# Optimization experiments

Measured on AMD Instinct MI355X. Metric: run time of the kernel, lower is better.

## Reference

```python
import jax, jax.numpy as jnp
import numpy as np

B, T, E, D, N, L, NF = 4, 2048, 512, 512, 16, 4, 2048


def setup_inputs() -> dict:
    key = jax.random.key(0)
    ks = jax.random.split(key, 12)
    r = lambda k, s, sc=1.0: jax.random.normal(k, s, dtype=jnp.float32) * sc
    return {
        "text_emb": r(ks[0], (B, T, E)),
        "W_in": r(ks[1], (E, D), 1.0 / np.sqrt(E).astype(np.float32)),
        "b_in": jnp.zeros((D,), jnp.float32),
        "freq_pe": r(ks[2], (NF, D), 0.02),
        # diagonal-SSM (S4D) params per layer, stacked on leading L axis
        "A_log": r(ks[3], (L, D, N), 0.5),
        "B_ssm": r(ks[4], (L, D, N), 0.5),
        "C_ssm": r(ks[5], (L, D, N), 0.5),
        "log_dt": r(ks[6], (L, D), 0.5) - 4.6,  # dt ~ 0.01
        "D_skip": r(ks[7], (L, D), 0.5),
        "ln_f0_scale": jnp.ones((D,), jnp.float32),
        "ln_f0_bias": jnp.zeros((D,), jnp.float32),
        "W_f0": r(ks[8], (D, 1), 1.0 / np.sqrt(D).astype(np.float32)),
        "b_f0": jnp.zeros((1,), jnp.float32),
        "ln_en_scale": jnp.ones((D,), jnp.float32),
        "ln_en_bias": jnp.zeros((D,), jnp.float32),
        "W_en": r(ks[9], (D, 1), 1.0 / np.sqrt(D).astype(np.float32)),
        "b_en": jnp.zeros((1,), jnp.float32),
    }


def _layernorm(x, scale, bias, eps=1e-5):
    mu = jnp.mean(x, axis=-1, keepdims=True)
    var = jnp.mean(jnp.square(x - mu), axis=-1, keepdims=True)
    return (x - mu) * jax.lax.rsqrt(var + eps) * scale + bias


def _s4_layer(h, A_log, Bm, Cm, log_dt, Dsk):
    # h: [B, T, D]; diagonal SSM with ZOH discretization, scanned over T.
    dt = jnp.exp(log_dt)                 # [D]
    A = -jnp.exp(A_log)                  # [D, N], stable (negative real)
    Abar = jnp.exp(dt[:, None] * A)      # [D, N]
    Bbar = (Abar - 1.0) / A * Bm         # [D, N]
    u_t = jnp.transpose(h, (1, 0, 2))    # [T, B, D]
    x0 = jnp.zeros((h.shape[0], h.shape[2], A.shape[1]), h.dtype)  # [B, D, N]

    def step(x, u):
        x = Abar * x + Bbar * u[..., None]          # [B, D, N]
        y = jnp.einsum('bdn,dn->bd', x, Cm)         # readout
        return x, y

    _, ys = jax.lax.scan(step, x0, u_t)             # ys: [T, B, D]
    y = jnp.transpose(ys, (1, 0, 2)) + Dsk * h      # D skip connection
    return h + jax.nn.gelu(y)                       # residual + activation


def _forward(text_emb, W_in, b_in, freq_pe, A_log, B_ssm, C_ssm, log_dt,
             D_skip, ln_f0_scale, ln_f0_bias, W_f0, b_f0,
             ln_en_scale, ln_en_bias, W_en, b_en):
    x = text_emb @ W_in + b_in                      # [B, T, D]
    Tlen = x.shape[1]
    nf = freq_pe.shape[0]
    if nf >= Tlen:                                  # static-shape crop
        freq = freq_pe[:Tlen]
    else:                                           # static-shape edge pad
        pad = jnp.repeat(freq_pe[-1:], Tlen - nf, axis=0)
        freq = jnp.concatenate([freq_pe, pad], axis=0)
    h = x + freq[None, :, :]
    for l in range(A_log.shape[0]):
        h = _s4_layer(h, A_log[l], B_ssm[l], C_ssm[l], log_dt[l], D_skip[l])
    f0 = (_layernorm(h, ln_f0_scale, ln_f0_bias) @ W_f0 + b_f0)[..., 0]
    en = (_layernorm(h, ln_en_scale, ln_en_bias) @ W_en + b_en)[..., 0]
    return f0, en


def reference(text_emb, W_in, b_in, freq_pe, A_log, B_ssm, C_ssm, log_dt,
              D_skip, ln_f0_scale, ln_f0_bias, W_f0, b_f0,
              ln_en_scale, ln_en_bias, W_en, b_en):
    return _forward(text_emb, W_in, b_in, freq_pe, A_log, B_ssm, C_ssm,
                    log_dt, D_skip, ln_f0_scale, ln_f0_bias, W_f0, b_f0,
                    ln_en_scale, ln_en_bias, W_en, b_en)
```

## Files before the change

### kernel.cpp

```cpp
#include <hip/hip_runtime.h>

#define B_   4
#define T_   2048
#define E_   512
#define D_   512
#define N_   16
#define L_   4
#define TCH  16

typedef __bf16 bf16x8 __attribute__((ext_vector_type(8)));
typedef float  f32x4  __attribute__((ext_vector_type(4)));
typedef float  f32x2  __attribute__((ext_vector_type(2)));
typedef unsigned short us8 __attribute__((ext_vector_type(8)));

__device__ __forceinline__ float us2f(unsigned short u) {
    return __uint_as_float(((unsigned int)u) << 16);
}
__device__ __forceinline__ unsigned short f2us(float f) {
    unsigned int u = __float_as_uint(f);
    unsigned int r = (u + 0x7fffu + ((u >> 16) & 1u)) >> 16;
    return (unsigned short)r;
}
__device__ __forceinline__ float ldin(const void* p, int i, unsigned int f) {
    return f ? ((const float*)p)[i] : us2f(((const unsigned short*)p)[i]);
}
__device__ __forceinline__ unsigned int probe_f32(const void* lnfs) {
    return (((const unsigned int*)lnfs)[0] == 0x3F800000u) ? 1u : 0u;
}
__device__ __forceinline__ f32x2 pk_fma(f32x2 a, f32x2 b, f32x2 c) {
    f32x2 d;
    asm("v_pk_fma_f32 %0, %1, %2, %3" : "=v"(d) : "v"(a), "v"(b), "v"(c));
    return d;
}
__device__ __forceinline__ f32x2 pk_mul(f32x2 a, f32x2 b) {
    f32x2 d;
    asm("v_pk_mul_f32 %0, %1, %2" : "=v"(d) : "v"(a), "v"(b));
    return d;
}
template<int CTRL, int RM>
__device__ __forceinline__ f32x2 dpp2(f32x2 v) {
    f32x2 r;
    r[0] = __int_as_float(__builtin_amdgcn_update_dpp(0, __float_as_int(v[0]), CTRL, RM, 0xF, true));
    r[1] = __int_as_float(__builtin_amdgcn_update_dpp(0, __float_as_int(v[1]), CTRL, RM, 0xF, true));
    return r;
}

#define PA    0
#define PB    32768
#define PC    65536
#define PDT   98304
#define PDSK  100352
#define PLFS  102400
#define PLFB  102912
#define PWF   103424
#define PLES  103936
#define PLEB  104448
#define PWEN  104960
#define PSC   105472
#define PRM_N 105474

#define NB_TEXT 2048
#define NB_PRM  413
#define NB_WT   64
#define NB_S4P  128

__global__ __launch_bounds__(256) void prep_kernel(
    const void* X, const void* Win,
    const void* A_log, const void* B_ssm, const void* C_ssm,
    const void* log_dt, const void* D_skip,
    const void* lnfs, const void* lnfb, const void* Wf0,
    const void* lnes, const void* lneb, const void* Wen,
    const void* bf0, const void* ben,
    unsigned short* __restrict__ textc, unsigned short* __restrict__ Wt,
    float* __restrict__ P, float* __restrict__ P2) {
    __shared__ float tile[64 * 65];
    unsigned int f = probe_f32(lnfs);
    int bid = blockIdx.x;
    if (bid < NB_TEXT) {
        int i = (bid * 256 + threadIdx.x) * 8;
        if (f) {
            const float* xf = (const float*)X;
            us8 r;
#pragma unroll
            for (int j = 0; j < 8; j++) r[j] = f2us(xf[i + j]);
            *(us8*)(textc + i) = r;
        } else {
            *(us8*)(textc + i) = *(const us8*)((const unsigned short*)X + i);
        }
    } else if (bid < NB_TEXT + NB_PRM) {
        int i = (bid - NB_TEXT) * 256 + threadIdx.x;
        if      (i < PB)     P[i] = ldin(A_log,  i - PA,   f);
        else if (i < PC)     P[i] = ldin(B_ssm,  i - PB,   f);
        else if (i < PDT)    P[i] = ldin(C_ssm,  i - PC,   f);
        else if (i < PDSK)   P[i] = ldin(log_dt, i - PDT,  f);
        else if (i < PLFS)   P[i] = ldin(D_skip, i - PDSK, f);
        else if (i < PLFB)   P[i] = ldin(lnfs,   i - PLFS, f);
        else if (i < PWF)    P[i] = ldin(lnfb,   i - PLFB, f);
        else if (i < PLES)   P[i] = ldin(Wf0,    i - PWF,  f);
        else if (i < PLEB)   P[i] = ldin(lnes,   i - PLES, f);
        else if (i < PWEN)   P[i] = ldin(lneb,   i - PLEB, f);
        else if (i < PSC)    P[i] = ldin(Wen,    i - PWEN, f);
        else if (i == PSC)     P[i] = ldin(bf0, 0, f);
        else if (i == PSC + 1) P[i] = ldin(ben, 0, f);
    } else if (bid < NB_TEXT + NB_PRM + NB_WT) {
        int tb = bid - (NB_TEXT + NB_PRM);
        int d0 = (tb >> 3) * 64, e0 = (tb & 7) * 64;
        int r = threadIdx.x >> 6, i = threadIdx.x & 63;
#pragma unroll
        for (int k = 0; k < 16; k++) {
            int e = k * 4 + r;
            tile[e * 65 + i] = ldin(Win, (e0 + e) * D_ + d0 + i, f);
        }
        __syncthreads();
#pragma unroll
        for (int k = 0; k < 16; k++) {
            int dd = k * 4 + r;
            Wt[(size_t)(d0 + dd) * E_ + e0 + i] = f2us(tile[i * 65 + dd]);
        }
    } else {
        int i = (bid - (NB_TEXT + NB_PRM + NB_WT)) * 256 + threadIdx.x;
        int n = i & 15;
        int ld = i >> 4;
        float dt = __expf(ldin(log_dt, ld, f));
        float A  = -__expf(ldin(A_log, i, f));
        float Ab = __expf(dt * A);
        float Bb = (Ab - 1.f) / A * ldin(B_ssm, i, f);
        float l2M = 23.083120654223414f * dt * A;
        int base = ld * 64 + n;
        P2[base]      = Ab;
        P2[base + 16] = Bb * ldin(C_ssm, i, f);
        P2[base + 32] = exp2f(l2M);
        P2[base + 48] = l2M;
    }
}

__global__ __launch_bounds__(256) void gemm_kernel(const unsigned short* __restrict__ X,
                                                   const unsigned short* __restrict__ Wt,
                                                   const void* __restrict__ freq,
                                                   const void* __restrict__ b_in,
                                                   const void* __restrict__ lnfs,
                                                   float* __restrict__ H) {
    __shared__ unsigned short wlds[64 * 264];
    const unsigned int fl = probe_f32(lnfs);
    const int tid = threadIdx.x;
    const int w  = tid >> 6;
    const int ln = tid & 15;
    const int q  = (tid >> 4) & 3;
    const int d0 = blockIdx.x * 64;
    const int t0 = blockIdx.y * 128;
    const int b  = blockIdx.z;

    f32x4 acc[2][4];
#pragma unroll
    for (int i = 0; i < 2; i++)
#pragma unroll
        for (int j = 0; j < 4; j++) { acc[i][j][0]=0.f; acc[i][j][1]=0.f; acc[i][j][2]=0.f; acc[i][j][3]=0.f; }

    const size_t xbase = ((size_t)b * T_ + t0) * E_;

#pragma unroll
    for (int p = 0; p < 2; ++p) {
        if (p) __syncthreads();
#pragma unroll
        for (int it = 0; it < 8; ++it) {
            int flat = it * 256 + tid;
            int d = flat >> 5;
            int e = (flat & 31) << 3;
            bf16x8 v = *(const bf16x8*)(Wt + (size_t)(d0 + d) * E_ + p * 256 + e);
            *(bf16x8*)(wlds + d * 264 + e) = v;
        }
        __syncthreads();
#pragma unroll
        for (int s = 0; s < 8; ++s) {
            const int eo = s * 32 + q * 8;
            bf16x8 bfr[4];
#pragma unroll
            for (int j = 0; j < 4; j++)
                bfr[j] = *(const bf16x8*)(wlds + (j * 16 + ln) * 264 + eo);
#pragma unroll
            for (int sub = 0; sub < 2; ++sub) {
                const int t = w * 32 + sub * 16 + ln;
                bf16x8 afr = *(const bf16x8*)(X + xbase + (size_t)t * E_ + p * 256 + eo);
#pragma unroll
                for (int j = 0; j < 4; j++)
                    acc[sub][j] = __builtin_amdgcn_mfma_f32_16x16x32_bf16(afr, bfr[j], acc[sub][j], 0, 0, 0);
            }
        }
    }
#pragma unroll
    for (int sub = 0; sub < 2; ++sub) {
#pragma unroll
        for (int j = 0; j < 4; j++) {
            int d  = d0 + j * 16 + ln;
            int tb = t0 + w * 32 + sub * 16 + q * 4;
            float bi = ldin(b_in, d, fl);
            f32x4 o;
#pragma unroll
            for (int r4 = 0; r4 < 4; r4++)
                o[r4] = acc[sub][j][r4] + ldin(freq, (tb + r4) * D_ + d, fl) + bi;
            *(f32x4*)(H + ((size_t)b * D_ + d) * T_ + tb) = o;
        }
    }
}

__global__ __launch_bounds__(256) __attribute__((amdgpu_waves_per_eu(4, 4)))
void s4_kernel(float* __restrict__ H, const float* __restrict__ P,
               const float* __restrict__ P2) {
    __shared__ float hstate[2][2][16];
    const int w = threadIdx.x >> 6, lane = threadIdx.x & 63;
    const int rp = w >> 1, half = w & 1;
    const int row = blockIdx.x * 2 + rp;
    const int d = row & (D_ - 1);
    float* gp = H + (size_t)row * T_ + half * 1024 + lane * TCH;

    float u[TCH];
#pragma unroll
    for (int k = 0; k < 4; k++) {
        f32x4 v = *(const f32x4*)(gp + k * 4);
        u[k * 4] = v[0]; u[k * 4 + 1] = v[1]; u[k * 4 + 2] = v[2]; u[k * 4 + 3] = v[3];
    }

    for (int l = 0; l < L_; ++l) {
        const float* pp = P2 + (size_t)(((l << 9) + d) << 6);
        f32x2 Ab[8];
#pragma unroll
        for (int n = 0; n < 8; n++) Ab[n] = *(const f32x2*)(pp + 2 * n);
        f32x2 b[8];
#pragma unroll
        for (int n = 0; n < 8; n++) { b[n][0] = 0.f; b[n][1] = 0.f; }
#pragma unroll
        for (int j = 0; j < TCH; j++) {
            f32x2 u2; u2[0] = u[j]; u2[1] = u[j];
#pragma unroll
            for (int n = 0; n < 8; n++) b[n] = pk_fma(Ab[n], b[n], u2);
        }
        {
            f32x2 M1[8], w1[8], w2[8];
            float e1 = (float)((lane & 15) + 1);
            bool hi16 = (lane & 16) != 0;
#pragma unroll
            for (int n = 0; n < 8; n++) {
                M1[n] = *(const f32x2*)(pp + 32 + 2 * n);
                f32x2 l2m = *(const f32x2*)(pp + 48 + 2 * n);
                w1[n][0] = exp2f(l2m[0] * e1);  w1[n][1] = exp2f(l2m[1] * e1);
            }
#pragma unroll
            for (int n = 0; n < 8; n++) b[n] = pk_fma(M1[n], dpp2<0x111, 0xF>(b[n]), b[n]);
#pragma unroll
            for (int n = 0; n < 8; n++) M1[n] = pk_mul(M1[n], M1[n]);
#pragma unroll
            for (int n = 0; n < 8; n++) b[n] = pk_fma(M1[n], dpp2<0x112, 0xF>(b[n]), b[n]);
#pragma unroll
            for (int n = 0; n < 8; n++) M1[n] = pk_mul(M1[n], M1[n]);
#pragma unroll
            for (int n = 0; n < 8; n++) b[n] = pk_fma(M1[n], dpp2<0x114, 0xF>(b[n]), b[n]);
#pragma unroll
            for (int n = 0; n < 8; n++) M1[n] = pk_mul(M1[n], M1[n]);
#pragma unroll
            for (int n = 0; n < 8; n++) b[n] = pk_fma(M1[n], dpp2<0x118, 0xF>(b[n]), b[n]);
#pragma unroll
            for (int n = 0; n < 8; n++) {
                f32x2 M16 = pk_mul(M1[n], M1[n]);
                f32x2 wm  = pk_mul(w1[n], M16);
                w2[n][0] = hi16 ? wm[0] : w1[n][0];
                w2[n][1] = hi16 ? wm[1] : w1[n][1];
            }
#pragma unroll
            for (int n = 0; n < 8; n++) b[n] = pk_fma(w1[n], dpp2<0x142, 0xA>(b[n]), b[n]);
#pragma unroll
            for (int n = 0; n < 8; n++) b[n] = pk_fma(w2[n], dpp2<0x143, 0xC>(b[n]), b[n]);
        }
        if (half == 0 && lane == 63) {
#pragma unroll
            for (int n = 0; n < 8; n++) {
                hstate[rp][l & 1][2 * n]     = b[n][0];
                hstate[rp][l & 1][2 * n + 1] = b[n][1];
            }
        }
        f32x2 z[8];
#pragma unroll
        for (int n = 0; n < 8; n++) {
            z[n][0] = __shfl_up(b[n][0], 1u, 64);
            z[n][1] = __shfl_up(b[n][1], 1u, 64);
            if (lane == 0) { z[n][0] = 0.f; z[n][1] = 0.f; }
        }
        __syncthreads();
        if (half) {
            float el = (float)lane;
            const float* hs = hstate[rp][l & 1];
#pragma unroll
            for (int n = 0; n < 8; n++) {
                f32x2 l2m = *(const f32x2*)(pp + 48 + 2 * n);
                f32x2 wh; wh[0] = exp2f(l2m[0] * el); wh[1] = exp2f(l2m[1] * el);
                f32x2 h0; h0[0] = hs[2 * n]; h0[1] = hs[2 * n + 1];
                z[n] = pk_fma(wh, h0, z[n]);
            }
        }
        float Dsk = P[PDSK + l * D_ + d];
        f32x2 CB[8];
#pragma unroll
        for (int n = 0; n < 8; n++) CB[n] = *(const f32x2*)(pp + 16 + 2 * n);
#pragma unroll
        for (int j = 0; j < TCH; j++) {
            float uu = u[j];
            f32x2 u2; u2[0] = uu; u2[1] = uu;
#pragma unroll
            for (int n = 0; n < 8; n++) z[n] = pk_fma(Ab[n], z[n], u2);
            f32x2 ya; ya[0] = 0.f; ya[1] = 0.f;
            f32x2 yb; yb[0] = 0.f; yb[1] = 0.f;
#pragma unroll
            for (int n = 0; n < 8; n += 2) {
                ya = pk_fma(CB[n], z[n], ya);
                yb = pk_fma(CB[n + 1], z[n + 1], yb);
            }
            f32x2 s = ya + yb;
            float y = fmaf(Dsk, uu, s[0] + s[1]);
            float zin = 0.7978845608028654f * fmaf(0.044715f, y * y * y, y);
            float e2  = __expf(2.f * zin);
            float r   = __builtin_amdgcn_rcpf(e2 + 1.f);
            u[j] = (uu + y) - y * r;
        }
    }
#pragma unroll
    for (int k = 0; k < 4; k++) {
        f32x4 v;
        v[0] = u[k * 4]; v[1] = u[k * 4 + 1]; v[2] = u[k * 4 + 2]; v[3] = u[k * 4 + 3];
        *(f32x4*)(gp + k * 4) = v;
    }
}

__global__ __launch_bounds__(256) void final_kernel(const float* __restrict__ H,
                                                    const float* __restrict__ P,
                                                    void* __restrict__ out,
                                                    const void* __restrict__ lnfs_raw) {
    __shared__ float red[4][8][64];
    unsigned int f = probe_f32(lnfs_raw);
    int tid = threadIdx.x;
    int w = tid >> 6, tl = tid & 63;
    int tg = blockIdx.x * 64 + tl;
    int b = tg >> 11, t = tg & (T_ - 1);
    float S1=0.f,S2=0.f,Pf=0.f,Pe=0.f,Cf=0.f,Ce=0.f,Df=0.f,De=0.f;
    const float* hp = H + ((size_t)b * D_) * T_ + t;
#pragma unroll 4
    for (int i = 0; i < 128; i++) {
        int d = w * 128 + i;
        float hv = hp[(size_t)d * T_];
        float sf = P[PLFS + d], bfv = P[PLFB + d], wf = P[PWF + d];
        float se = P[PLES + d], bev = P[PLEB + d], we = P[PWEN + d];
        S1 += hv; S2 = fmaf(hv, hv, S2);
        float tf = sf * wf, te = se * we;
        Pf = fmaf(hv, tf, Pf); Pe = fmaf(hv, te, Pe);
        Cf += tf; Ce += te;
        Df = fmaf(bfv, wf, Df); De = fmaf(bev, we, De);
    }
    red[w][0][tl]=S1; red[w][1][tl]=S2; red[w][2][tl]=Pf; red[w][3][tl]=Pe;
    red[w][4][tl]=Cf; red[w][5][tl]=Ce; red[w][6][tl]=Df; red[w][7][tl]=De;
    __syncthreads();
    if (w == 0) {
        float a[8];
#pragma unroll
        for (int k = 0; k < 8; k++)
            a[k] = red[0][k][tl] + red[1][k][tl] + red[2][k][tl] + red[3][k][tl];
        float mu  = a[0] * (1.f / 512.f);
        float var = a[1] * (1.f / 512.f) - mu * mu;
        float r   = rsqrtf(var + 1e-5f);
        float f0  = r * (a[2] - mu * a[4]) + a[6] + P[PSC + 0];
        float en  = r * (a[3] - mu * a[5]) + a[7] + P[PSC + 1];
        if (f) {
            ((float*)out)[tg]           = f0;
            ((float*)out)[B_ * T_ + tg] = en;
        } else {
            ((unsigned short*)out)[tg]           = f2us(f0);
            ((unsigned short*)out)[B_ * T_ + tg] = f2us(en);
        }
    }
}

extern "C" void kernel_launch(void* const* d_in, const int* in_sizes, int n_in,
                              void* d_out, int out_size, void* d_ws, size_t ws_size,
                              hipStream_t stream) {
    (void)in_sizes; (void)n_in; (void)out_size; (void)ws_size;
    float* ws = (float*)d_ws;
    float* P     = ws;
    float* H     = ws + 105504;
    unsigned short* textc = (unsigned short*)(ws + 4299808);
    unsigned short* Wt    = (unsigned short*)(ws + 6396960);
    float* P2    = ws + 6528032;

    prep_kernel<<<dim3(NB_TEXT + NB_PRM + NB_WT + NB_S4P), dim3(256), 0, stream>>>(
        d_in[0], d_in[1], d_in[4], d_in[5], d_in[6], d_in[7], d_in[8],
        d_in[9], d_in[10], d_in[11], d_in[13], d_in[14], d_in[15],
        d_in[12], d_in[16], textc, Wt, P, P2);
    gemm_kernel<<<dim3(8, 16, 4), dim3(256), 0, stream>>>(textc, Wt, d_in[3], d_in[2], d_in[9], H);
    s4_kernel<<<dim3(1024), dim3(256), 0, stream>>>(H, P, P2);
    final_kernel<<<dim3(128), dim3(256), 0, stream>>>(H, P, d_out, d_in[9]);
}
```

Baseline: 178.1 us.

## Precompute decay power table, halve s4 block size, use DPP shift and sigmoid GELU

The prep kernel now writes a per-(layer,d,n) table of M^1..M^16 so the s4 kernel loads the w1 weights instead of computing exp2f per lane. The s4 kernel runs one row per 128-thread block instead of two rows per 256-thread block, which gives finer barrier granularity. The shfl_up is replaced by a DPP row-shift, and GELU is rewritten as y*sigmoid via exp2 with the residual folded into one fma. The wh exponentials and parameter loads are hoisted before the barrier to overlap with it. In exchange there is an extra 2 MB workspace table and additional global loads.

```diff
diff --git a/kernel.cpp b/kernel.cpp
--- a/kernel.cpp
+++ b/kernel.cpp
@@ -72,7 +72,7 @@
     const void* lnes, const void* lneb, const void* Wen,
     const void* bf0, const void* ben,
     unsigned short* __restrict__ textc, unsigned short* __restrict__ Wt,
-    float* __restrict__ P, float* __restrict__ P2) {
+    float* __restrict__ P, float* __restrict__ P2, float* __restrict__ P3) {
     __shared__ float tile[64 * 65];
     unsigned int f = probe_f32(lnfs);
     int bid = blockIdx.x;
@@ -126,11 +126,16 @@
         float Ab = __expf(dt * A);
         float Bb = (Ab - 1.f) / A * ldin(B_ssm, i, f);
         float l2M = 23.083120654223414f * dt * A;
+        float M   = exp2f(l2M);
         int base = ld * 64 + n;
         P2[base]      = Ab;
         P2[base + 16] = Bb * ldin(C_ssm, i, f);
-        P2[base + 32] = exp2f(l2M);
+        P2[base + 32] = M;
         P2[base + 48] = l2M;
+        float pw = M;
+        size_t pb = ((size_t)ld << 8) + n;
+#pragma unroll
+        for (int k = 0; k < 16; k++) { P3[pb + k * 16] = pw; pw *= M; }
     }
 }
 
@@ -203,13 +208,12 @@
     }
 }
 
-__global__ __launch_bounds__(256) __attribute__((amdgpu_waves_per_eu(4, 4)))
+__global__ __launch_bounds__(128) __attribute__((amdgpu_waves_per_eu(4, 4)))
 void s4_kernel(float* __restrict__ H, const float* __restrict__ P,
-               const float* __restrict__ P2) {
-    __shared__ float hstate[2][2][16];
-    const int w = threadIdx.x >> 6, lane = threadIdx.x & 63;
-    const int rp = w >> 1, half = w & 1;
-    const int row = blockIdx.x * 2 + rp;
+               const float* __restrict__ P2, const float* __restrict__ P3) {
+    __shared__ float hstate[2][16];
+    const int half = threadIdx.x >> 6, lane = threadIdx.x & 63;
+    const int row = blockIdx.x;
     const int d = row & (D_ - 1);
     float* gp = H + (size_t)row * T_ + half * 1024 + lane * TCH;
 
@@ -222,9 +226,12 @@
 
     for (int l = 0; l < L_; ++l) {
         const float* pp = P2 + (size_t)(((l << 9) + d) << 6);
-        f32x2 Ab[8];
+        const float* pw = P3 + ((size_t)((l << 9) + d) << 8) + ((lane & 15) << 4);
+        f32x2 Ab[8], w1[8];
 #pragma unroll
         for (int n = 0; n < 8; n++) Ab[n] = *(const f32x2*)(pp + 2 * n);
+#pragma unroll
+        for (int n = 0; n < 8; n++) w1[n] = *(const f32x2*)(pw + 2 * n);
         f32x2 b[8];
 #pragma unroll
         for (int n = 0; n < 8; n++) { b[n][0] = 0.f; b[n][1] = 0.f; }
@@ -235,29 +242,24 @@
             for (int n = 0; n < 8; n++) b[n] = pk_fma(Ab[n], b[n], u2);
         }
         {
-            f32x2 M1[8], w1[8], w2[8];
-            float e1 = (float)((lane & 15) + 1);
+            f32x2 M1[8], w2[8];
+#pragma unroll
+            for (int n = 0; n < 8; n++) M1[n] = *(const f32x2*)(pp + 32 + 2 * n);
+#pragma unroll
+            for (int n = 0; n < 8; n++) b[n] = pk_fma(M1[n], dpp2<0x111, 0xF>(b[n]), b[n]);
+#pragma unroll
+            for (int n = 0; n < 8; n++) M1[n] = pk_mul(M1[n], M1[n]);
+#pragma unroll
+            for (int n = 0; n < 8; n++) b[n] = pk_fma(M1[n], dpp2<0x112, 0xF>(b[n]), b[n]);
+#pragma unroll
+            for (int n = 0; n < 8; n++) M1[n] = pk_mul(M1[n], M1[n]);
+#pragma unroll
+            for (int n = 0; n < 8; n++) b[n] = pk_fma(M1[n], dpp2<0x114, 0xF>(b[n]), b[n]);
+#pragma unroll
+            for (int n = 0; n < 8; n++) M1[n] = pk_mul(M1[n], M1[n]);
+#pragma unroll
+            for (int n = 0; n < 8; n++) b[n] = pk_fma(M1[n], dpp2<0x118, 0xF>(b[n]), b[n]);
             bool hi16 = (lane & 16) != 0;
-#pragma unroll
-            for (int n = 0; n < 8; n++) {
-                M1[n] = *(const f32x2*)(pp + 32 + 2 * n);
-                f32x2 l2m = *(const f32x2*)(pp + 48 + 2 * n);
-                w1[n][0] = exp2f(l2m[0] * e1);  w1[n][1] = exp2f(l2m[1] * e1);
-            }
-#pragma unroll
-            for (int n = 0; n < 8; n++) b[n] = pk_fma(M1[n], dpp2<0x111, 0xF>(b[n]), b[n]);
-#pragma unroll
-            for (int n = 0; n < 8; n++) M1[n] = pk_mul(M1[n], M1[n]);
-#pragma unroll
-            for (int n = 0; n < 8; n++) b[n] = pk_fma(M1[n], dpp2<0x112, 0xF>(b[n]), b[n]);
-#pragma unroll
-            for (int n = 0; n < 8; n++) M1[n] = pk_mul(M1[n], M1[n]);
-#pragma unroll
-            for (int n = 0; n < 8; n++) b[n] = pk_fma(M1[n], dpp2<0x114, 0xF>(b[n]), b[n]);
-#pragma unroll
-            for (int n = 0; n < 8; n++) M1[n] = pk_mul(M1[n], M1[n]);
-#pragma unroll
-            for (int n = 0; n < 8; n++) b[n] = pk_fma(M1[n], dpp2<0x118, 0xF>(b[n]), b[n]);
 #pragma unroll
             for (int n = 0; n < 8; n++) {
                 f32x2 M16 = pk_mul(M1[n], M1[n]);
@@ -270,36 +272,39 @@
 #pragma unroll
             for (int n = 0; n < 8; n++) b[n] = pk_fma(w2[n], dpp2<0x143, 0xC>(b[n]), b[n]);
         }
+        f32x2 wh[8];
+        if (half) {
+            float el = (float)lane;
+#pragma unroll
+            for (int n = 0; n < 8; n++) {
+                f32x2 l2m = *(const f32x2*)(pp + 48 + 2 * n);
+                wh[n][0] = exp2f(l2m[0] * el);
+                wh[n][1] = exp2f(l2m[1] * el);
+            }
+        }
+        float Dsk = P[PDSK + l * D_ + d];
+        f32x2 CB[8];
+#pragma unroll
+        for (int n = 0; n < 8; n++) CB[n] = *(const f32x2*)(pp + 16 + 2 * n);
         if (half == 0 && lane == 63) {
 #pragma unroll
             for (int n = 0; n < 8; n++) {
-                hstate[rp][l & 1][2 * n]     = b[n][0];
-                hstate[rp][l & 1][2 * n + 1] = b[n][1];
+                hstate[l & 1][2 * n]     = b[n][0];
+                hstate[l & 1][2 * n + 1] = b[n][1];
             }
         }
         f32x2 z[8];
 #pragma unroll
-        for (int n = 0; n < 8; n++) {
-            z[n][0] = __shfl_up(b[n][0], 1u, 64);
-            z[n][1] = __shfl_up(b[n][1], 1u, 64);
-            if (lane == 0) { z[n][0] = 0.f; z[n][1] = 0.f; }
-        }
+        for (int n = 0; n < 8; n++) z[n] = dpp2<0x138, 0xF>(b[n]);
         __syncthreads();
         if (half) {
-            float el = (float)lane;
-            const float* hs = hstate[rp][l & 1];
+            const float* hs = hstate[l & 1];
 #pragma unroll
             for (int n = 0; n < 8; n++) {
-                f32x2 l2m = *(const f32x2*)(pp + 48 + 2 * n);
-                f32x2 wh; wh[0] = exp2f(l2m[0] * el); wh[1] = exp2f(l2m[1] * el);
                 f32x2 h0; h0[0] = hs[2 * n]; h0[1] = hs[2 * n + 1];
-                z[n] = pk_fma(wh, h0, z[n]);
-            }
-        }
-        float Dsk = P[PDSK + l * D_ + d];
-        f32x2 CB[8];
-#pragma unroll
-        for (int n = 0; n < 8; n++) CB[n] = *(const f32x2*)(pp + 16 + 2 * n);
+                z[n] = pk_fma(wh[n], h0, z[n]);
+            }
+        }
 #pragma unroll
         for (int j = 0; j < TCH; j++) {
             float uu = u[j];
@@ -315,10 +320,10 @@
             }
             f32x2 s = ya + yb;
             float y = fmaf(Dsk, uu, s[0] + s[1]);
-            float zin = 0.7978845608028654f * fmaf(0.044715f, y * y * y, y);
-            float e2  = __expf(2.f * zin);
-            float r   = __builtin_amdgcn_rcpf(e2 + 1.f);
-            u[j] = (uu + y) - y * r;
+            float t  = fmaf(0.044715f, y * y * y, y);
+            float em = exp2f(-2.30220818f * t);
+            float r  = __builtin_amdgcn_rcpf(1.f + em);
+            u[j] = fmaf(y, r, uu);
         }
     }
 #pragma unroll
@@ -386,12 +391,13 @@
     unsigned short* textc = (unsigned short*)(ws + 4299808);
     unsigned short* Wt    = (unsigned short*)(ws + 6396960);
     float* P2    = ws + 6528032;
+    float* P3    = ws + 6659104;
 
     prep_kernel<<<dim3(NB_TEXT + NB_PRM + NB_WT + NB_S4P), dim3(256), 0, stream>>>(
         d_in[0], d_in[1], d_in[4], d_in[5], d_in[6], d_in[7], d_in[8],
         d_in[9], d_in[10], d_in[11], d_in[13], d_in[14], d_in[15],
-        d_in[12], d_in[16], textc, Wt, P, P2);
+        d_in[12], d_in[16], textc, Wt, P, P2, P3);
     gemm_kernel<<<dim3(8, 16, 4), dim3(256), 0, stream>>>(textc, Wt, d_in[3], d_in[2], d_in[9], H);
-    s4_kernel<<<dim3(1024), dim3(256), 0, stream>>>(H, P, P2);
+    s4_kernel<<<dim3(2048), dim3(128), 0, stream>>>(H, P, P2, P3);
     final_kernel<<<dim3(128), dim3(256), 0, stream>>>(H, P, d_out, d_in[9]);
 }
```

Result: faster. 173.4 us (-2.6%).
